# Performance work log

Hardware: AMD Instinct MI355X
Metric: run time of the kernel (lower is better)

The kernel has to match this reference:

```python
import jax, jax.numpy as jnp
import numpy as np

N = 100000          # total nodes
E = 1200000         # total edges
IN_CH = 22          # NUM_NODES_SINGLE_TEAM * 2
HID = 64
NUM_CLASSES = 3
G = 256             # graphs in batch


def setup_inputs() -> dict:
    key = jax.random.key(0)
    ks = jax.random.split(key, 12)
    x = jax.random.normal(ks[0], (N, IN_CH), jnp.float32)
    edge_index = jax.random.randint(ks[1], (2, E), 0, N, dtype=jnp.int32)
    edge_weight = jax.random.uniform(ks[2], (E,), jnp.float32)
    batch = jnp.sort(jax.random.randint(ks[3], (N,), 0, G, dtype=jnp.int32))

    def lin_w(k, fi, fo):
        return jax.random.normal(k, (fi, fo), jnp.float32) / np.float32(np.sqrt(fi))

    return {
        "x": x,
        "edge_index": edge_index,
        "edge_weight": edge_weight,
        "batch": batch,
        "W1": lin_w(ks[4], IN_CH, HID),  "b1": jnp.zeros((HID,), jnp.float32),
        "W2": lin_w(ks[5], HID, HID),    "b2": jnp.zeros((HID,), jnp.float32),
        "fw1": lin_w(ks[6], HID, HID),   "fb1": jnp.zeros((HID,), jnp.float32),
        "fw2": lin_w(ks[7], HID, NUM_CLASSES), "fb2": jnp.zeros((NUM_CLASSES,), jnp.float32),
    }


def gcn_conv(x, edge_index, edge_weight, W, b):
    """PyG GCNConv: self-loops (weight 1) + symmetric normalization + scatter-add."""
    n = x.shape[0]
    loop = jnp.arange(n, dtype=edge_index.dtype)
    row = jnp.concatenate([edge_index[0], loop])
    col = jnp.concatenate([edge_index[1], loop])
    w = jnp.concatenate([edge_weight, jnp.ones((n,), x.dtype)])
    deg = jax.ops.segment_sum(w, col, num_segments=n)        # weighted in-degree
    safe = jnp.where(deg > 0, deg, 1.0)
    dinv = jnp.where(deg > 0, jax.lax.rsqrt(safe), 0.0)
    norm = dinv[row] * w * dinv[col]                         # [E+N]
    h = x @ W                                                # transform first (d small)
    msg = norm[:, None] * h[row]                             # gather + scale
    out = jax.ops.segment_sum(msg, col, num_segments=n)      # scatter-add
    return out + b


def reference(x, edge_index, edge_weight, batch, W1, b1, W2, b2, fw1, fb1, fw2, fb2):
    h = jax.nn.relu(gcn_conv(x, edge_index, edge_weight, W1, b1))
    h = jax.nn.relu(gcn_conv(h, edge_index, edge_weight, W2, b2))
    # global_mean_pool
    sums = jax.ops.segment_sum(h, batch, num_segments=G)
    cnt = jax.ops.segment_sum(jnp.ones((h.shape[0],), h.dtype), batch, num_segments=G)
    pooled = sums / jnp.maximum(cnt, 1.0)[:, None]
    h = jax.nn.relu(pooled @ fw1 + fb1)
    return h @ fw2 + fb2
```

## Files before the change

### kernel.cpp

```cpp
#include <hip/hip_runtime.h>
#include <hip/hip_bf16.h>
#include <hip/hip_fp16.h>


#define HIDC 64
#define MTILE 128
#define XS_STRIDE (MTILE + 4)
#define BSHIFT 9
#define SPAN 512
#define NBKT_MAX 256
#define BCHUNK 2048

typedef unsigned long long u64;

__global__ void k_init(int* bucket_cnt, int nb, float* pooled, int npool) {
    int i = blockIdx.x * blockDim.x + threadIdx.x;
    if (i < nb) bucket_cnt[i] = 0;
    if (i < npool) pooled[i] = 0.f;
}

__global__ __launch_bounds__(256) void k_bin_count(const int* __restrict__ col,
                                                   int* bucket_cnt, int E, int NB) {
    __shared__ int hist[NBKT_MAX];
    int tid = threadIdx.x;
    for (int i = tid; i < NB; i += 256) hist[i] = 0;
    __syncthreads();
    int base = blockIdx.x * 8192;
    for (int j = 0; j < 32; ++j) {
        int e = base + j * 256 + tid;
        if (e < E) atomicAdd(&hist[col[e] >> BSHIFT], 1);
    }
    __syncthreads();
    for (int i = tid; i < NB; i += 256)
        if (hist[i]) atomicAdd(&bucket_cnt[i], hist[i]);
}

__global__ void k_bucket_scan(const int* __restrict__ bucket_cnt, int* __restrict__ bucket_base,
                              int* __restrict__ cursor_g, int NB, int E) {
    __shared__ int s[256];
    int t = threadIdx.x;
    int v = (t < NB) ? bucket_cnt[t] : 0;
    s[t] = v;
    __syncthreads();
    for (int o = 1; o < 256; o <<= 1) {
        int x = (t >= o) ? s[t - o] : 0;
        __syncthreads();
        s[t] += x;
        __syncthreads();
    }
    if (t < NB) { int ex = s[t] - v; bucket_base[t] = ex; cursor_g[t] = ex; }
    if (t == 0) bucket_base[NB] = E;
}

__global__ __launch_bounds__(256) void k_bin_scatter(const int* __restrict__ row,
                                                     const int* __restrict__ col,
                                                     const float* __restrict__ ew,
                                                     int* cursor_g, u64* __restrict__ bedges,
                                                     int E, int NB) {
    __shared__ int hist[NBKT_MAX], binoff[NBKT_MAX], cursor[NBKT_MAX], gbase[NBKT_MAX];
    __shared__ int s[256];
    __shared__ u64 stage[BCHUNK];
    __shared__ unsigned char binid[BCHUNK];
    int tid = threadIdx.x;
    for (int i = tid; i < NB; i += 256) hist[i] = 0;
    __syncthreads();
    int base = blockIdx.x * BCHUNK;
    u64 pk[8]; int bb[8];
#pragma unroll
    for (int j = 0; j < 8; ++j) {
        int e = base + j * 256 + tid;
        if (e < E) {
            int c = col[e];
            bb[j] = c >> BSHIFT;
            pk[j] = ((u64)__float_as_uint(ew[e]) << 32) |
                    ((u64)(unsigned)row[e] << BSHIFT) | (unsigned)(c & (SPAN - 1));
            atomicAdd(&hist[bb[j]], 1);
        } else bb[j] = -1;
    }
    __syncthreads();
    {
        int v = (tid < NB) ? hist[tid] : 0;
        s[tid] = v;
        __syncthreads();
        for (int o = 1; o < 256; o <<= 1) {
            int x = (tid >= o) ? s[tid - o] : 0;
            __syncthreads();
            s[tid] += x;
            __syncthreads();
        }
        if (tid < NB) { binoff[tid] = s[tid] - v; cursor[tid] = s[tid] - v; }
    }
    __syncthreads();
#pragma unroll
    for (int j = 0; j < 8; ++j)
        if (bb[j] >= 0) {
            int pos = atomicAdd(&cursor[bb[j]], 1);
            stage[pos] = pk[j];
            binid[pos] = (unsigned char)bb[j];
        }
    __syncthreads();
    if (tid < NB && hist[tid] > 0) gbase[tid] = atomicAdd(&cursor_g[tid], hist[tid]);
    __syncthreads();
    int total = min(BCHUNK, E - base);
    for (int i = tid; i < total; i += 256) {
        int b = binid[i];
        bedges[(size_t)gbase[b] + (i - binoff[b])] = stage[i];
    }
}

__global__ __launch_bounds__(256) void k_bucket_process(const u64* __restrict__ bedges,
                                                        const int* __restrict__ bucket_base,
                                                        u64* __restrict__ csr,
                                                        float* __restrict__ dinv,
                                                        int* __restrict__ off,
                                                        int N, int E, int NB) {
    __shared__ float deg[SPAN];
    __shared__ int cL[SPAN];
    __shared__ int offL[SPAN];
    __shared__ int s[256];
    int b = blockIdx.x, tid = threadIdx.x;
    int ebase = bucket_base[b], ecnt = bucket_base[b + 1] - ebase;
    int nd0 = b << BSHIFT;
    int ndn = min(SPAN, N - nd0);
    for (int i = tid; i < SPAN; i += 256) { deg[i] = 1.0f; cL[i] = 0; }
    __syncthreads();
    for (int e = tid; e < ecnt; e += 256) {
        u64 p = bedges[ebase + e];
        int colin = (int)(p & (SPAN - 1));
        atomicAdd(&deg[colin], __uint_as_float((unsigned)(p >> 32)));
        atomicAdd(&cL[colin], 1);
    }
    __syncthreads();
    int p0 = cL[2 * tid], p1 = cL[2 * tid + 1];
    s[tid] = p0 + p1;
    __syncthreads();
    for (int o = 1; o < 256; o <<= 1) {
        int x = (tid >= o) ? s[tid - o] : 0;
        __syncthreads();
        s[tid] += x;
        __syncthreads();
    }
    int ex = s[tid] - (p0 + p1);
    offL[2 * tid] = ex;
    offL[2 * tid + 1] = ex + p0;
    __syncthreads();
    for (int i = tid; i < ndn; i += 256) {
        dinv[nd0 + i] = rsqrtf(deg[i]);
        off[nd0 + i] = ebase + offL[i];
    }
    for (int i = tid; i < SPAN; i += 256) cL[i] = offL[i];
    if (b == NB - 1 && tid == 0) off[N] = E;
    __syncthreads();
    for (int e = tid; e < ecnt; e += 256) {
        u64 p = bedges[ebase + e];
        int colin = (int)(p & (SPAN - 1));
        int src = (int)((p >> BSHIFT) & 0x7FFFFF);
        int slot = atomicAdd(&cL[colin], 1);
        csr[(size_t)ebase + slot] = ((u64)(unsigned)src << 32) | (unsigned)(p >> 32);
    }
}

__global__ void k_prep_x16(const float* __restrict__ x, const float* __restrict__ dinv,
                           __half* __restrict__ x16, int n, int K) {
    int t = blockIdx.x * blockDim.x + threadIdx.x;
    int node = t >> 4, p = t & 15;
    if (node >= n) return;
    int c0 = p * 2;
    float d = dinv[node];
    float a = (c0 < K)     ? d * x[(size_t)node * K + c0]     : 0.f;
    float b = (c0 + 1 < K) ? d * x[(size_t)node * K + c0 + 1] : 0.f;
    reinterpret_cast<__half2*>(x16)[(size_t)node * 16 + p] = __floats2half2_rn(a, b);
}

__global__ void k_agg_x(const __half* __restrict__ x16, const int* __restrict__ off,
                        const u64* __restrict__ csr, const float* __restrict__ dinv,
                        float* __restrict__ agg, int n, int K) {
    int t = blockIdx.x * blockDim.x + threadIdx.x;
    int lane = threadIdx.x & 63;
    int node = ((t >> 6) << 3) + (lane >> 3);
    int sub = lane & 7;
    if (node >= n) return;
    const uint2* xp = reinterpret_cast<const uint2*>(x16);
    uint2 sv = xp[(size_t)node * 8 + sub];
    float acc0, acc1, acc2, acc3;
    {
        float2 a = __half22float2(*(const __half2*)&sv.x);
        float2 b = __half22float2(*(const __half2*)&sv.y);
        acc0 = a.x; acc1 = a.y; acc2 = b.x; acc3 = b.y;
    }
    int i = off[node], e1 = off[node + 1];
    for (; i + 7 < e1; i += 8) {
        u64 e[8]; uint2 r[8];
#pragma unroll
        for (int j = 0; j < 8; ++j) e[j] = csr[i + j];
#pragma unroll
        for (int j = 0; j < 8; ++j) r[j] = xp[(size_t)(e[j] >> 32) * 8 + sub];
#pragma unroll
        for (int j = 0; j < 8; ++j) {
            float w = __uint_as_float((unsigned)e[j]);
            float2 a = __half22float2(*(const __half2*)&r[j].x);
            float2 b = __half22float2(*(const __half2*)&r[j].y);
            acc0 = fmaf(w, a.x, acc0); acc1 = fmaf(w, a.y, acc1);
            acc2 = fmaf(w, b.x, acc2); acc3 = fmaf(w, b.y, acc3);
        }
    }
    for (; i < e1; ++i) {
        u64 e0 = csr[i];
        uint2 r = xp[(size_t)(e0 >> 32) * 8 + sub];
        float w = __uint_as_float((unsigned)e0);
        float2 a = __half22float2(*(const __half2*)&r.x);
        float2 b = __half22float2(*(const __half2*)&r.y);
        acc0 = fmaf(w, a.x, acc0); acc1 = fmaf(w, a.y, acc1);
        acc2 = fmaf(w, b.x, acc2); acc3 = fmaf(w, b.y, acc3);
    }
    int c0 = sub * 4;
    float d = dinv[node];
    float* ap = agg + (size_t)node * K + c0;
    if (c0 + 3 < K) {
        float2 o0; o0.x = d * acc0; o0.y = d * acc1;
        float2 o1; o1.x = d * acc2; o1.y = d * acc3;
        *reinterpret_cast<float2*>(ap) = o0;
        *reinterpret_cast<float2*>(ap + 2) = o1;
    } else if (c0 < K) {
        float2 o; o.x = d * acc0; o.y = d * acc1;
        *reinterpret_cast<float2*>(ap) = o;
    }
}

template <int K1>
__global__ __launch_bounds__(256) void k_layer1_fused(const float* __restrict__ agg,
                                                      const float* __restrict__ W1,
                                                      const float* __restrict__ b1,
                                                      const float* __restrict__ W2,
                                                      const float* __restrict__ dinv,
                                                      __half* __restrict__ h, int n) {
    __shared__ float smem[HIDC * XS_STRIDE];
    __shared__ float ws[HIDC * HIDC];
    int tid = threadIdx.x;
    int n0 = blockIdx.x * MTILE;

    for (int i = tid; i < K1 * HIDC; i += 256) ws[i] = W1[i];
    for (int i = tid; i < MTILE * K1; i += 256) {
        int r = i / K1, k = i - r * K1;
        smem[k * XS_STRIDE + r] = (n0 + r < n) ? agg[(size_t)(n0 + r) * K1 + k] : 0.f;
    }
    __syncthreads();

    int c0 = (tid & 15) * 4;
    int m0 = (tid >> 4) * 8;
    float acc[8][4];
#pragma unroll
    for (int j = 0; j < 8; ++j)
#pragma unroll
        for (int q = 0; q < 4; ++q) acc[j][q] = 0.f;

#pragma unroll 2
    for (int k = 0; k < K1; ++k) {
        float4 a0 = *reinterpret_cast<const float4*>(&smem[k * XS_STRIDE + m0]);
        float4 a1 = *reinterpret_cast<const float4*>(&smem[k * XS_STRIDE + m0 + 4]);
        float4 b  = *reinterpret_cast<const float4*>(&ws[k * HIDC + c0]);
        float av[8] = {a0.x, a0.y, a0.z, a0.w, a1.x, a1.y, a1.z, a1.w};
        float bv[4] = {b.x, b.y, b.z, b.w};
#pragma unroll
        for (int j = 0; j < 8; ++j)
#pragma unroll
            for (int q = 0; q < 4; ++q)
                acc[j][q] = fmaf(av[j], bv[q], acc[j][q]);
    }

    float4 bb = *reinterpret_cast<const float4*>(b1 + c0);
    float bv4[4] = {bb.x, bb.y, bb.z, bb.w};
#pragma unroll
    for (int j = 0; j < 8; ++j)
#pragma unroll
        for (int q = 0; q < 4; ++q)
            acc[j][q] = fmaxf(acc[j][q] + bv4[q], 0.f);

    __syncthreads();

#pragma unroll
    for (int j = 0; j < 8; ++j)
#pragma unroll
        for (int q = 0; q < 4; ++q)
            smem[(c0 + q) * XS_STRIDE + (m0 + j)] = (n0 + m0 + j < n) ? acc[j][q] : 0.f;
    for (int i = tid; i < HIDC * HIDC; i += 256) ws[i] = W2[i];
    __syncthreads();

#pragma unroll
    for (int j = 0; j < 8; ++j)
#pragma unroll
        for (int q = 0; q < 4; ++q) acc[j][q] = 0.f;

#pragma unroll 2
    for (int k = 0; k < HIDC; ++k) {
        float4 a0 = *reinterpret_cast<const float4*>(&smem[k * XS_STRIDE + m0]);
        float4 a1 = *reinterpret_cast<const float4*>(&smem[k * XS_STRIDE + m0 + 4]);
        float4 b  = *reinterpret_cast<const float4*>(&ws[k * HIDC + c0]);
        float av[8] = {a0.x, a0.y, a0.z, a0.w, a1.x, a1.y, a1.z, a1.w};
        float bv[4] = {b.x, b.y, b.z, b.w};
#pragma unroll
        for (int j = 0; j < 8; ++j)
#pragma unroll
            for (int q = 0; q < 4; ++q)
                acc[j][q] = fmaf(av[j], bv[q], acc[j][q]);
    }

#pragma unroll
    for (int j = 0; j < 8; ++j) {
        int node = n0 + m0 + j;
        if (node < n) {
            float dv = dinv[node];
            union { struct { __half2 a, b; } h2; float2 f2; } u;
            u.h2.a = __floats2half2_rn(acc[j][0] * dv, acc[j][1] * dv);
            u.h2.b = __floats2half2_rn(acc[j][2] * dv, acc[j][3] * dv);
            *reinterpret_cast<float2*>(h + (size_t)node * HIDC + c0) = u.f2;
        }
    }
}

__global__ void k_gcn_gather(const __half* __restrict__ h, const int* __restrict__ off,
                             const u64* __restrict__ csr, const float* __restrict__ dinv,
                             const float* __restrict__ bias, float* __restrict__ out, int n) {
    int t = blockIdx.x * blockDim.x + threadIdx.x;
    int lane = threadIdx.x & 63;
    int node = ((t >> 6) << 2) + (lane >> 4);
    int sub = lane & 15;
    if (node >= n) return;
    const uint2* hp = reinterpret_cast<const uint2*>(h);
    float d = dinv[node];
    uint2 sv = hp[(size_t)node * 16 + sub];
    float acc0, acc1, acc2, acc3;
    {
        float2 a = __half22float2(*(const __half2*)&sv.x);
        float2 b = __half22float2(*(const __half2*)&sv.y);
        acc0 = a.x; acc1 = a.y; acc2 = b.x; acc3 = b.y;
    }
    int i = off[node], e1 = off[node + 1];
    for (; i + 7 < e1; i += 8) {
        u64 e[8]; uint2 r[8];
#pragma unroll
        for (int j = 0; j < 8; ++j) e[j] = csr[i + j];
#pragma unroll
        for (int j = 0; j < 8; ++j) r[j] = hp[(size_t)(e[j] >> 32) * 16 + sub];
#pragma unroll
        for (int j = 0; j < 8; ++j) {
            float w = __uint_as_float((unsigned)e[j]);
            float2 a = __half22float2(*(const __half2*)&r[j].x);
            float2 b = __half22float2(*(const __half2*)&r[j].y);
            acc0 = fmaf(w, a.x, acc0); acc1 = fmaf(w, a.y, acc1);
            acc2 = fmaf(w, b.x, acc2); acc3 = fmaf(w, b.y, acc3);
        }
    }
    for (; i < e1; ++i) {
        u64 e0 = csr[i];
        uint2 r = hp[(size_t)(e0 >> 32) * 16 + sub];
        float w = __uint_as_float((unsigned)e0);
        float2 a = __half22float2(*(const __half2*)&r.x);
        float2 b = __half22float2(*(const __half2*)&r.y);
        acc0 = fmaf(w, a.x, acc0); acc1 = fmaf(w, a.y, acc1);
        acc2 = fmaf(w, b.x, acc2); acc3 = fmaf(w, b.y, acc3);
    }
    int c0 = sub * 4;
    float4 bb = *reinterpret_cast<const float4*>(bias + c0);
    float4 o;
    o.x = fmaxf(fmaf(d, acc0, bb.x), 0.f);
    o.y = fmaxf(fmaf(d, acc1, bb.y), 0.f);
    o.z = fmaxf(fmaf(d, acc2, bb.z), 0.f);
    o.w = fmaxf(fmaf(d, acc3, bb.w), 0.f);
    *reinterpret_cast<float4*>(out + (size_t)node * HIDC + c0) = o;
}

__global__ void k_pool(const float* __restrict__ h, const int* __restrict__ batch,
                       float* __restrict__ pooled, float* __restrict__ cnt, int n) {
    int c = threadIdx.x & 63, sub = threadIdx.x >> 6;
    int n0 = blockIdx.x * 256;
    int nend = min(n0 + 256, n);
    float acc = 0.f, cacc = 0.f;
    int curb = -1;
    for (int i = n0 + sub; i < nend; i += 4) {
        int b = batch[i];
        if (b != curb) {
            if (curb >= 0) {
                atomicAdd(&pooled[curb * HIDC + c], acc);
                if (c == 0) atomicAdd(&cnt[curb], cacc);
            }
            acc = 0.f; cacc = 0.f;
            curb = b;
        }
        acc += h[(size_t)i * HIDC + c];
        cacc += 1.f;
    }
    if (curb >= 0) {
        atomicAdd(&pooled[curb * HIDC + c], acc);
        if (c == 0) atomicAdd(&cnt[curb], cacc);
    }
}

__global__ void k_head(const float* __restrict__ pooled, const float* __restrict__ cnt,
                       const float* __restrict__ fw1, const float* __restrict__ fb1,
                       const float* __restrict__ fw2, const float* __restrict__ fb2,
                       float* __restrict__ out, int nclass) {
    int g = blockIdx.x;
    int j = threadIdx.x;
    __shared__ float p[HIDC], hid[HIDC];
    float c = fmaxf(cnt[g], 1.0f);
    p[j] = pooled[g * HIDC + j] / c;
    __syncthreads();
    float acc = fb1[j];
#pragma unroll 8
    for (int k = 0; k < HIDC; ++k) acc = fmaf(p[k], fw1[k * HIDC + j], acc);
    hid[j] = fmaxf(acc, 0.f);
    __syncthreads();
    if (j < nclass) {
        float o = fb2[j];
#pragma unroll 8
        for (int k = 0; k < HIDC; ++k) o = fmaf(hid[k], fw2[k * nclass + j], o);
        out[g * nclass + j] = o;
    }
}

extern "C" void kernel_launch(void* const* d_in, const int* in_sizes, int n_in,
                              void* d_out, int out_size, void* d_ws, size_t ws_size,
                              hipStream_t stream) {
    const float* x    = (const float*)d_in[0];
    const int* eidx   = (const int*)d_in[1];
    const float* ew   = (const float*)d_in[2];
    const int* batch  = (const int*)d_in[3];
    const float* W1   = (const float*)d_in[4];
    const float* b1   = (const float*)d_in[5];
    const float* W2   = (const float*)d_in[6];
    const float* b2   = (const float*)d_in[7];
    const float* fw1  = (const float*)d_in[8];
    const float* fb1  = (const float*)d_in[9];
    const float* fw2  = (const float*)d_in[10];
    const float* fb2  = (const float*)d_in[11];
    float* out = (float*)d_out;

    const int N = in_sizes[3];
    const int E = in_sizes[1] / 2;
    const int INCH = in_sizes[0] / N;
    const int NCLASS = in_sizes[11];
    const int G = out_size / NCLASS;
    const int NB = (N + SPAN - 1) >> BSHIFT;

    const int* row = eidx;
    const int* col = eidx + E;

    char* wp = (char*)d_ws;
    u64*   bedges = (u64*)wp;    wp += sizeof(u64) * E;
    u64*   csr    = (u64*)wp;    wp += sizeof(u64) * E;
    float* dinv   = (float*)wp;  wp += sizeof(float) * N;
    __half* x16   = (__half*)wp; wp += sizeof(__half) * (size_t)N * 32;
    float* agg    = (float*)wp;  wp += sizeof(float) * (size_t)N * INCH;
    __half* hbuf  = (__half*)wp; wp += sizeof(__half) * (size_t)N * HIDC;
    float* bufB   = (float*)wp;  wp += sizeof(float) * (size_t)N * HIDC;
    float* pooled = (float*)wp;  wp += sizeof(float) * (size_t)G * HIDC;
    float* cnt    = (float*)wp;  wp += sizeof(float) * G;
    int*   off    = (int*)wp;    wp += sizeof(int) * (N + 1);
    int*   bucket_cnt  = (int*)wp; wp += sizeof(int) * NBKT_MAX;
    int*   bucket_base = (int*)wp; wp += sizeof(int) * (NBKT_MAX + 1);
    int*   cursor_g    = (int*)wp; wp += sizeof(int) * NBKT_MAX;

    const int BLK = 256;
    dim3 blk(BLK);
    int gTile   = (N + MTILE - 1) / MTILE;
    int gGather = (N + 15) / 16;
    int gAggX   = (N + 31) / 32;
    int gPrep   = ((size_t)N * 16 + BLK - 1) / BLK;
    int nInit   = max(NB, G * HIDC + G);

    k_init<<<(nInit + BLK - 1) / BLK, blk, 0, stream>>>(bucket_cnt, NB, pooled, G * HIDC + G);

    k_bin_count<<<(E + 8191) / 8192, blk, 0, stream>>>(col, bucket_cnt, E, NB);
    k_bucket_scan<<<1, blk, 0, stream>>>(bucket_cnt, bucket_base, cursor_g, NB, E);
    k_bin_scatter<<<(E + BCHUNK - 1) / BCHUNK, blk, 0, stream>>>(row, col, ew, cursor_g,
                                                                 bedges, E, NB);
    k_bucket_process<<<NB, blk, 0, stream>>>(bedges, bucket_base, csr, dinv, off, N, E, NB);

    k_prep_x16<<<gPrep, blk, 0, stream>>>(x, dinv, x16, N, INCH);
    k_agg_x<<<gAggX, blk, 0, stream>>>(x16, off, csr, dinv, agg, N, INCH);
    k_layer1_fused<22><<<gTile, blk, 0, stream>>>(agg, W1, b1, W2, dinv, hbuf, N);

    k_gcn_gather<<<gGather, blk, 0, stream>>>(hbuf, off, csr, dinv, b2, bufB, N);

    k_pool<<<(N + 255) / 256, blk, 0, stream>>>(bufB, batch, pooled, cnt, N);
    k_head<<<G, dim3(64), 0, stream>>>(pooled, cnt, fw1, fb1, fw2, fb2, out, NCLASS);
}
```

Measured before the change: 193.0 us.

## Fuse layer-2 gather with mean pooling and fold x16 prep into bucket processing

The layer-2 neighbor gather now reduces its ReLU outputs straight into per-block shared-memory segment sums keyed by graph id, then flushes them to the pooled buffer with global atomics. This removes the N×64 fp32 intermediate write and read and the separate pool kernel. Separately, the half-precision x prep (scaling x by dinv) moves into the tail of k_bucket_process, using dinv already held in shared memory, which saves a launch and a dinv reload. The cost is extra shared-memory atomics, fallback global atomics when a block spans more than four graphs, and extra serial work in the bucket kernel, which has few blocks.

```diff
diff --git a/kernel.cpp b/kernel.cpp
--- a/kernel.cpp
+++ b/kernel.cpp
@@ -10,6 +10,7 @@
 #define SPAN 512
 #define NBKT_MAX 256
 #define BCHUNK 2048
+#define MAXSEG 4
 
 typedef unsigned long long u64;
 
@@ -110,10 +111,12 @@
 
 __global__ __launch_bounds__(256) void k_bucket_process(const u64* __restrict__ bedges,
                                                         const int* __restrict__ bucket_base,
+                                                        const float* __restrict__ x,
                                                         u64* __restrict__ csr,
                                                         float* __restrict__ dinv,
                                                         int* __restrict__ off,
-                                                        int N, int E, int NB) {
+                                                        __half* __restrict__ x16,
+                                                        int N, int E, int NB, int K) {
     __shared__ float deg[SPAN];
     __shared__ int cL[SPAN];
     __shared__ int offL[SPAN];
@@ -135,9 +138,9 @@
     s[tid] = p0 + p1;
     __syncthreads();
     for (int o = 1; o < 256; o <<= 1) {
-        int x = (tid >= o) ? s[tid - o] : 0;
+        int x_ = (tid >= o) ? s[tid - o] : 0;
         __syncthreads();
-        s[tid] += x;
+        s[tid] += x_;
         __syncthreads();
     }
     int ex = s[tid] - (p0 + p1);
@@ -145,7 +148,9 @@
     offL[2 * tid + 1] = ex + p0;
     __syncthreads();
     for (int i = tid; i < ndn; i += 256) {
-        dinv[nd0 + i] = rsqrtf(deg[i]);
+        float dv = rsqrtf(deg[i]);
+        deg[i] = dv;
+        dinv[nd0 + i] = dv;
         off[nd0 + i] = ebase + offL[i];
     }
     for (int i = tid; i < SPAN; i += 256) cL[i] = offL[i];
@@ -158,18 +163,14 @@
         int slot = atomicAdd(&cL[colin], 1);
         csr[(size_t)ebase + slot] = ((u64)(unsigned)src << 32) | (unsigned)(p >> 32);
     }
-}
-
-__global__ void k_prep_x16(const float* __restrict__ x, const float* __restrict__ dinv,
-                           __half* __restrict__ x16, int n, int K) {
-    int t = blockIdx.x * blockDim.x + threadIdx.x;
-    int node = t >> 4, p = t & 15;
-    if (node >= n) return;
-    int c0 = p * 2;
-    float d = dinv[node];
-    float a = (c0 < K)     ? d * x[(size_t)node * K + c0]     : 0.f;
-    float b = (c0 + 1 < K) ? d * x[(size_t)node * K + c0 + 1] : 0.f;
-    reinterpret_cast<__half2*>(x16)[(size_t)node * 16 + p] = __floats2half2_rn(a, b);
+    for (int i = tid; i < ndn * 16; i += 256) {
+        int nl = i >> 4, p = i & 15, c0 = p * 2;
+        float dv = deg[nl];
+        const float* xr = x + (size_t)(nd0 + nl) * K;
+        float a = (c0 < K)     ? dv * xr[c0]     : 0.f;
+        float bq = (c0 + 1 < K) ? dv * xr[c0 + 1] : 0.f;
+        reinterpret_cast<__half2*>(x16)[(size_t)(nd0 + nl) * 16 + p] = __floats2half2_rn(a, bq);
+    }
 }
 
 __global__ void k_agg_x(const __half* __restrict__ x16, const int* __restrict__ off,
@@ -318,81 +319,95 @@
     }
 }
 
-__global__ void k_gcn_gather(const __half* __restrict__ h, const int* __restrict__ off,
-                             const u64* __restrict__ csr, const float* __restrict__ dinv,
-                             const float* __restrict__ bias, float* __restrict__ out, int n) {
-    int t = blockIdx.x * blockDim.x + threadIdx.x;
-    int lane = threadIdx.x & 63;
-    int node = ((t >> 6) << 2) + (lane >> 4);
+__global__ __launch_bounds__(512) void k_gather_pool(const __half* __restrict__ h,
+                                                     const int* __restrict__ off,
+                                                     const u64* __restrict__ csr,
+                                                     const float* __restrict__ dinv,
+                                                     const float* __restrict__ bias,
+                                                     const int* __restrict__ batch,
+                                                     float* __restrict__ pooled,
+                                                     float* __restrict__ cnt, int n) {
+    __shared__ float segsum[MAXSEG][HIDC];
+    __shared__ int segcnt[MAXSEG];
+    __shared__ int sbase;
+    int tid = threadIdx.x;
+    int lane = tid & 63;
+    int nodeInBlk = ((tid >> 6) << 2) + (lane >> 4);
+    int node = blockIdx.x * 32 + nodeInBlk;
     int sub = lane & 15;
-    if (node >= n) return;
-    const uint2* hp = reinterpret_cast<const uint2*>(h);
-    float d = dinv[node];
-    uint2 sv = hp[(size_t)node * 16 + sub];
-    float acc0, acc1, acc2, acc3;
-    {
-        float2 a = __half22float2(*(const __half2*)&sv.x);
-        float2 b = __half22float2(*(const __half2*)&sv.y);
-        acc0 = a.x; acc1 = a.y; acc2 = b.x; acc3 = b.y;
-    }
-    int i = off[node], e1 = off[node + 1];
-    for (; i + 7 < e1; i += 8) {
-        u64 e[8]; uint2 r[8];
-#pragma unroll
-        for (int j = 0; j < 8; ++j) e[j] = csr[i + j];
-#pragma unroll
-        for (int j = 0; j < 8; ++j) r[j] = hp[(size_t)(e[j] >> 32) * 16 + sub];
-#pragma unroll
-        for (int j = 0; j < 8; ++j) {
-            float w = __uint_as_float((unsigned)e[j]);
-            float2 a = __half22float2(*(const __half2*)&r[j].x);
-            float2 b = __half22float2(*(const __half2*)&r[j].y);
+    if (tid < MAXSEG * HIDC) segsum[tid >> 6][tid & 63] = 0.f;
+    if (tid < MAXSEG) segcnt[tid] = 0;
+    if (tid == 0) {
+        int i0 = (int)blockIdx.x * 32;
+        if (i0 > n - 1) i0 = n - 1;
+        sbase = batch[i0];
+    }
+    __syncthreads();
+
+    if (node < n) {
+        const uint2* hp = reinterpret_cast<const uint2*>(h);
+        float d = dinv[node];
+        uint2 sv = hp[(size_t)node * 16 + sub];
+        float acc0, acc1, acc2, acc3;
+        {
+            float2 a = __half22float2(*(const __half2*)&sv.x);
+            float2 b = __half22float2(*(const __half2*)&sv.y);
+            acc0 = a.x; acc1 = a.y; acc2 = b.x; acc3 = b.y;
+        }
+        int i = off[node], e1 = off[node + 1];
+        for (; i + 7 < e1; i += 8) {
+            u64 e[8]; uint2 r[8];
+#pragma unroll
+            for (int j = 0; j < 8; ++j) e[j] = csr[i + j];
+#pragma unroll
+            for (int j = 0; j < 8; ++j) r[j] = hp[(size_t)(e[j] >> 32) * 16 + sub];
+#pragma unroll
+            for (int j = 0; j < 8; ++j) {
+                float w = __uint_as_float((unsigned)e[j]);
+                float2 a = __half22float2(*(const __half2*)&r[j].x);
+                float2 b = __half22float2(*(const __half2*)&r[j].y);
+                acc0 = fmaf(w, a.x, acc0); acc1 = fmaf(w, a.y, acc1);
+                acc2 = fmaf(w, b.x, acc2); acc3 = fmaf(w, b.y, acc3);
+            }
+        }
+        for (; i < e1; ++i) {
+            u64 e0 = csr[i];
+            uint2 r = hp[(size_t)(e0 >> 32) * 16 + sub];
+            float w = __uint_as_float((unsigned)e0);
+            float2 a = __half22float2(*(const __half2*)&r.x);
+            float2 b = __half22float2(*(const __half2*)&r.y);
             acc0 = fmaf(w, a.x, acc0); acc1 = fmaf(w, a.y, acc1);
             acc2 = fmaf(w, b.x, acc2); acc3 = fmaf(w, b.y, acc3);
         }
-    }
-    for (; i < e1; ++i) {
-        u64 e0 = csr[i];
-        uint2 r = hp[(size_t)(e0 >> 32) * 16 + sub];
-        float w = __uint_as_float((unsigned)e0);
-        float2 a = __half22float2(*(const __half2*)&r.x);
-        float2 b = __half22float2(*(const __half2*)&r.y);
-        acc0 = fmaf(w, a.x, acc0); acc1 = fmaf(w, a.y, acc1);
-        acc2 = fmaf(w, b.x, acc2); acc3 = fmaf(w, b.y, acc3);
-    }
-    int c0 = sub * 4;
-    float4 bb = *reinterpret_cast<const float4*>(bias + c0);
-    float4 o;
-    o.x = fmaxf(fmaf(d, acc0, bb.x), 0.f);
-    o.y = fmaxf(fmaf(d, acc1, bb.y), 0.f);
-    o.z = fmaxf(fmaf(d, acc2, bb.z), 0.f);
-    o.w = fmaxf(fmaf(d, acc3, bb.w), 0.f);
-    *reinterpret_cast<float4*>(out + (size_t)node * HIDC + c0) = o;
-}
-
-__global__ void k_pool(const float* __restrict__ h, const int* __restrict__ batch,
-                       float* __restrict__ pooled, float* __restrict__ cnt, int n) {
-    int c = threadIdx.x & 63, sub = threadIdx.x >> 6;
-    int n0 = blockIdx.x * 256;
-    int nend = min(n0 + 256, n);
-    float acc = 0.f, cacc = 0.f;
-    int curb = -1;
-    for (int i = n0 + sub; i < nend; i += 4) {
-        int b = batch[i];
-        if (b != curb) {
-            if (curb >= 0) {
-                atomicAdd(&pooled[curb * HIDC + c], acc);
-                if (c == 0) atomicAdd(&cnt[curb], cacc);
-            }
-            acc = 0.f; cacc = 0.f;
-            curb = b;
-        }
-        acc += h[(size_t)i * HIDC + c];
-        cacc += 1.f;
-    }
-    if (curb >= 0) {
-        atomicAdd(&pooled[curb * HIDC + c], acc);
-        if (c == 0) atomicAdd(&cnt[curb], cacc);
+        int c0 = sub * 4;
+        float4 bb = *reinterpret_cast<const float4*>(bias + c0);
+        float o0 = fmaxf(fmaf(d, acc0, bb.x), 0.f);
+        float o1 = fmaxf(fmaf(d, acc1, bb.y), 0.f);
+        float o2 = fmaxf(fmaf(d, acc2, bb.z), 0.f);
+        float o3 = fmaxf(fmaf(d, acc3, bb.w), 0.f);
+        int g = batch[node];
+        int bl = g - sbase;
+        if (bl >= 0 && bl < MAXSEG) {
+            atomicAdd(&segsum[bl][c0 + 0], o0);
+            atomicAdd(&segsum[bl][c0 + 1], o1);
+            atomicAdd(&segsum[bl][c0 + 2], o2);
+            atomicAdd(&segsum[bl][c0 + 3], o3);
+            if (sub == 0) atomicAdd(&segcnt[bl], 1);
+        } else {
+            atomicAdd(&pooled[(size_t)g * HIDC + c0 + 0], o0);
+            atomicAdd(&pooled[(size_t)g * HIDC + c0 + 1], o1);
+            atomicAdd(&pooled[(size_t)g * HIDC + c0 + 2], o2);
+            atomicAdd(&pooled[(size_t)g * HIDC + c0 + 3], o3);
+            if (sub == 0) atomicAdd(&cnt[g], 1.f);
+        }
+    }
+    __syncthreads();
+    if (tid < MAXSEG * HIDC) {
+        int sgi = tid >> 6, c = tid & 63;
+        if (segcnt[sgi] > 0) {
+            atomicAdd(&pooled[(size_t)(sbase + sgi) * HIDC + c], segsum[sgi][c]);
+            if (c == 0) atomicAdd(&cnt[sbase + sgi], (float)segcnt[sgi]);
+        }
     }
 }
 
@@ -453,7 +468,6 @@
     __half* x16   = (__half*)wp; wp += sizeof(__half) * (size_t)N * 32;
     float* agg    = (float*)wp;  wp += sizeof(float) * (size_t)N * INCH;
     __half* hbuf  = (__half*)wp; wp += sizeof(__half) * (size_t)N * HIDC;
-    float* bufB   = (float*)wp;  wp += sizeof(float) * (size_t)N * HIDC;
     float* pooled = (float*)wp;  wp += sizeof(float) * (size_t)G * HIDC;
     float* cnt    = (float*)wp;  wp += sizeof(float) * G;
     int*   off    = (int*)wp;    wp += sizeof(int) * (N + 1);
@@ -464,9 +478,8 @@
     const int BLK = 256;
     dim3 blk(BLK);
     int gTile   = (N + MTILE - 1) / MTILE;
-    int gGather = (N + 15) / 16;
     int gAggX   = (N + 31) / 32;
-    int gPrep   = ((size_t)N * 16 + BLK - 1) / BLK;
+    int gGP     = (N + 31) / 32;
     int nInit   = max(NB, G * HIDC + G);
 
     k_init<<<(nInit + BLK - 1) / BLK, blk, 0, stream>>>(bucket_cnt, NB, pooled, G * HIDC + G);
@@ -475,14 +488,14 @@
     k_bucket_scan<<<1, blk, 0, stream>>>(bucket_cnt, bucket_base, cursor_g, NB, E);
     k_bin_scatter<<<(E + BCHUNK - 1) / BCHUNK, blk, 0, stream>>>(row, col, ew, cursor_g,
                                                                  bedges, E, NB);
-    k_bucket_process<<<NB, blk, 0, stream>>>(bedges, bucket_base, csr, dinv, off, N, E, NB);
-
-    k_prep_x16<<<gPrep, blk, 0, stream>>>(x, dinv, x16, N, INCH);
+    k_bucket_process<<<NB, blk, 0, stream>>>(bedges, bucket_base, x, csr, dinv, off, x16,
+                                             N, E, NB, INCH);
+
     k_agg_x<<<gAggX, blk, 0, stream>>>(x16, off, csr, dinv, agg, N, INCH);
     k_layer1_fused<22><<<gTile, blk, 0, stream>>>(agg, W1, b1, W2, dinv, hbuf, N);
 
-    k_gcn_gather<<<gGather, blk, 0, stream>>>(hbuf, off, csr, dinv, b2, bufB, N);
-
-    k_pool<<<(N + 255) / 256, blk, 0, stream>>>(bufB, batch, pooled, cnt, N);
+    k_gather_pool<<<gGP, dim3(512), 0, stream>>>(hbuf, off, csr, dinv, b2, batch,
+                                                 pooled, cnt, N);
+
     k_head<<<G, dim3(64), 0, stream>>>(pooled, cnt, fw1, fb1, fw2, fb2, out, NCLASS);
 }
```

After: 209.9 us. 8.8% more time.
